# Performance work log

Hardware: AMD Instinct MI355X
Metric: run time of the kernel (lower is better)

The kernel has to match this reference:

```python
import jax, jax.numpy as jnp
import numpy as np

THRESHOLD = 0.9
N = 20000
K = 32
F = 64


def setup_inputs() -> dict:
    key = jax.random.key(0)
    k1, k2, k3, k4, k5 = jax.random.split(key, 5)
    features = jax.random.normal(k1, (N, F), dtype=jnp.float32)
    score = jax.random.normal(k2, (N, 1), dtype=jnp.float32)
    distances = jax.random.uniform(k3, (N, K), dtype=jnp.float32)
    # two equal segments; neighbours sampled within own segment, self at col 0
    row_splits = jnp.array([0, N // 2, N], dtype=jnp.int32)
    segN = N // 2
    local_self = (jnp.arange(N, dtype=jnp.int32) % segN)
    seg_start = (jnp.arange(N, dtype=jnp.int32) // segN) * segN
    r = jax.random.randint(k4, (N, K - 1), 0, segN - 1, dtype=jnp.int32)
    r = r + (r >= local_self[:, None]).astype(jnp.int32)  # avoid sampling self
    neigh = seg_start[:, None] + r
    nidxs = jnp.concatenate([jnp.arange(N, dtype=jnp.int32)[:, None], neigh], axis=1)
    tidxs = jax.random.randint(k5, (N, 1), 0, 50, dtype=jnp.int32)
    return {"features": features, "score": score, "distances": distances,
            "nidxs": nidxs, "row_splits": row_splits, "tidxs": tidxs}


def _lnc(features, score_logits, nidxs, row_splits):
    n, k = nidxs.shape
    score = jax.nn.sigmoid(score_logits[:, 0])  # [N]
    # hierarchy order: per row-split segment, descending score
    seg_id = jnp.searchsorted(row_splits, jnp.arange(n), side='right') - 1
    order = jnp.lexsort((-score, seg_id))

    arangeK = jnp.arange(k)

    def step(carry, p):
        ggather, sel, npg, gcount = carry
        already = ggather[p] >= 0
        high = score[p] > THRESHOLD
        m = nidxs[p]                                   # [K], m[0] == p (self)
        free = (m >= 0) & (ggather[jnp.clip(m, 0, n - 1)] < 0)
        self_only = arangeK == 0
        valid = jnp.where(high, free, self_only) & (~already) & (m >= 0)
        g = gcount
        idx_w = jnp.where(valid, m, n)                 # dummy slot n for masked writes
        ggather = ggather.at[idx_w].set(g)
        row_i = jnp.where(already, n, g)
        sel = sel.at[row_i].set(jnp.where(valid, m, -1))
        npg = npg.at[row_i].set(jnp.sum(valid.astype(jnp.int32)))
        created = (~already).astype(jnp.int32)
        return (ggather, sel, npg, gcount + created), created

    init = (jnp.full((n + 1,), -1, jnp.int32),
            jnp.full((n + 1, k), -1, jnp.int32),
            jnp.zeros((n + 1,), jnp.int32),
            jnp.int32(0))
    (ggather, sel, npg, gcount), created = jax.lax.scan(step, init, order)
    ggather, sel, npg = ggather[:n], sel[:n], npg[:n]

    # new row splits: cumulative group count at segment boundaries
    cum = jnp.cumsum(created)
    rs_new = jnp.concatenate([jnp.zeros((1,), jnp.int32),
                              cum[row_splits[1:] - 1].astype(jnp.int32)])

    # pooled features per group (rows >= gcount are padding)
    sel_c = jnp.clip(sel, 0, n - 1)
    gathered = features[sel_c]                         # [N, K, F]
    mask = (sel >= 0)[..., None]
    out_mean = jnp.sum(jnp.where(mask, gathered, 0.0), axis=1)
    out_mean = out_mean / (npg[:, None].astype(features.dtype) + 1e-6)
    out_max = jnp.max(jnp.where(mask, gathered, -1000.0), axis=1)
    out = jnp.concatenate([out_mean, out_max], axis=-1)  # [N, 2F]
    backgather = ggather[:, None]
    return out, rs_new, backgather


def reference(features, score, distances, nidxs, row_splits, tidxs):
    # distances/tidxs only feed the (disabled) loss branch; kept for signature parity
    return _lnc(features, score, nidxs, row_splits)
```

## Files before the change

### kernel.cpp

```cpp
#include <hip/hip_runtime.h>


constexpr int KN = 32;
constexpr int FD = 64;
constexpr int HOCAP = 512;
constexpr int EW = 16;
constexpr int NBB = 2048;
constexpr int NT = 256;
constexpr int NMAX = 20000;
constexpr int BSLOT = 64;
constexpr int TS = 2048;

typedef unsigned long long u64;

__device__ __forceinline__ int swz(int i) { return i ^ ((i >> 4) & 3); }

__global__ void k0_init(const float* __restrict__ score, float* __restrict__ s,
                        int* __restrict__ grab, u64* __restrict__ hlkStage,
                        int* __restrict__ hcnt, int* __restrict__ lcnt0,
                        int* __restrict__ lcnt1, u64* __restrict__ key,
                        const int* __restrict__ row_splits, int n) {
  __shared__ int ch, cl0, cl1;
  int tid = (int)threadIdx.x, bid = (int)blockIdx.x;
  int x = bid * NT + tid;
  int lane = tid & 63;
  int half = row_splits[1];
  if (tid == 0) { ch = 0; cl0 = 0; cl1 = 0; }
  __syncthreads();
  bool hi = false, lo = false;
  u64 pk = 0;
  if (x < n) {
    float sp = 1.0f / (1.0f + expf(-score[x]));
    s[x] = sp; grab[x] = 0x7FFFFFFF;
    hi = sp > 0.9f; lo = !hi;
    unsigned sb = __float_as_uint(sp);
    pk = ((u64)(x >= half) << 63) | ((u64)(0x7FFFFFFFu - sb) << 32) | (unsigned)x;
    key[x] = lo ? (((u64)sb << 32) | (u64)(0xFFFFFFFFu - (unsigned)x)) : 0ull;
  }
  u64 bh = __ballot(hi);
  u64 b0 = __ballot(lo && x < half);
  u64 b1 = __ballot(lo && x >= half);
  int base = 0;
  if (lane == 0) {
    if (bh) base = atomicAdd(&ch, __popcll(bh));
    if (b0) atomicAdd(&cl0, __popcll(b0));
    if (b1) atomicAdd(&cl1, __popcll(b1));
  }
  base = __shfl(base, 0);
  if (hi) {
    int idx = base + __popcll(bh & ((1ull << lane) - 1ull));
    if (idx < BSLOT) hlkStage[bid * BSLOT + idx] = pk;
  }
  __syncthreads();
  if (tid == 0) {
    hcnt[bid] = (ch > BSLOT) ? BSLOT : ch;
    lcnt0[bid] = cl0; lcnt1[bid] = cl1;
  }
}

__global__ __launch_bounds__(1024, 1) void kA(
    const u64* __restrict__ hlkStage, const int* __restrict__ hcnt,
    const int* __restrict__ lcnt0, const int* __restrict__ lcnt1,
    const int* __restrict__ nidxs, const int* __restrict__ row_splits,
    int* __restrict__ nbm, int* __restrict__ fgj, int* __restrict__ counters,
    int n) {
  __shared__ unsigned short hr16[NMAX];
  __shared__ unsigned E[HOCAP * EW];
  __shared__ u64 hk[HOCAP];
  __shared__ int hol[HOCAP];
  __shared__ int fgjL[HOCAP];
  __shared__ int cnts[128];
  __shared__ int pref[129];
  __shared__ int lsum[2];
  __shared__ int shg;
  int tid = (int)threadIdx.x;
  int lane = tid & 63;
  int half = row_splits[1];
  int nblk = (n + NT - 1) / NT; if (nblk > 128) nblk = 128;

  {
    unsigned* h32 = (unsigned*)hr16;
    for (int i = tid; i < NMAX / 2; i += 1024) h32[i] = 0xFFFFFFFFu;
  }
  for (int i = tid; i < HOCAP * EW; i += 1024) E[i] = 0u;
  if (tid < 128) cnts[tid] = (tid < nblk) ? hcnt[tid] : 0;
  if (tid == 0) { lsum[0] = 0; lsum[1] = 0; }
  __syncthreads();

  if (tid < 64) {
    int v0 = cnts[tid], v1 = cnts[64 + tid];
#pragma unroll
    for (int off = 1; off < 64; off <<= 1) {
      int t0 = __shfl_up(v0, off), t1 = __shfl_up(v1, off);
      if (lane >= off) { v0 += t0; v1 += t1; }
    }
    int s0 = __shfl(v0, 63);
    pref[tid + 1] = v0;
    pref[64 + tid + 1] = v1 + s0;
    if (tid == 0) pref[0] = 0;
  }
  if (tid >= 64 && tid < 192) {
    int b = tid - 64;
    if (b < nblk) { atomicAdd(&lsum[0], lcnt0[b]); atomicAdd(&lsum[1], lcnt1[b]); }
  }
  __syncthreads();
  int nh = pref[nblk]; if (nh > HOCAP) nh = HOCAP;

  for (int t = tid; t < nblk * BSLOT; t += 1024) {
    int b = t >> 6, j = t & (BSLOT - 1);
    if (j < cnts[b]) {
      int d = pref[b] + j;
      if (d < HOCAP) hk[d] = hlkStage[t];
    }
  }
  __syncthreads();

  for (int i = tid; i < nh; i += 1024) {
    u64 kp = hk[i];
    int rk = 0;
#pragma unroll 8
    for (int j = 0; j < nh; ++j) rk += (hk[j] < kp) ? 1 : 0;
    int p = (int)(unsigned)(kp & 0xFFFFFFFFu);
    hol[rk] = p; hr16[p] = (unsigned short)rk;
  }
  __syncthreads();

  {
    const int4* nsrc = (const int4*)nidxs;
    int4* ndstG = (int4*)nbm;
    int tot = nh * 8;
    for (int t = tid; t < tot; t += 1024) {
      int j = t >> 3, q4 = t & 7;
      int p = hol[j];
      int4 v = nsrc[p * 8 + q4];
      ndstG[t] = v;
      unsigned bit = 1u << (j & 31);
      unsigned widx = (unsigned)(j >> 5);
      int xs[4] = { v.x, v.y, v.z, v.w };
#pragma unroll
      for (int e = 0; e < 4; ++e) {
        unsigned r = ((unsigned)xs[e] < (unsigned)n) ? hr16[xs[e]] : 0xFFFFu;
        if (r != 0xFFFFu) atomicOr(&E[r * EW + widx], bit);
      }
    }
  }
  __syncthreads();

  if (tid < 64) {
    unsigned Fw[16];
#pragma unroll
    for (int w = 0; w < 16; ++w) Fw[w] = 0u;
    int hg = 0, h0 = 0, h1 = 0;
    u64 mask_lt = (1ull << lane) - 1ull;
#pragma unroll
    for (int c = 0; c < HOCAP / 64; ++c) {
      if (c * 64 >= nh) break;
      int j = c * 64 + lane;
      bool valid = j < nh;
      unsigned er[16];
#pragma unroll
      for (int w = 0; w < 16; ++w) er[w] = valid ? E[j * EW + w] : 0u;
      unsigned acc = 0;
#pragma unroll
      for (int w = 0; w < 16; ++w) acc |= er[w] & Fw[w];
      bool base_already = acc != 0u;
      u64 erc = ((u64)er[2 * c + 1] << 32) | er[2 * c];
      u64 fb = 0;
      for (int l = 0; l < 64; ++l) {
        bool already = base_already || ((erc & fb) != 0ull);
        bool formed = valid && !already;
        fb |= __ballot(formed && (lane == l));
      }
      Fw[2 * c]     |= (unsigned)(fb & 0xFFFFFFFFull);
      Fw[2 * c + 1] |= (unsigned)(fb >> 32);
      bool formed = (fb >> lane) & 1ull;
      int p = valid ? hol[j] : 0;
      if (formed) {
        int idx = hg + __popcll(fb & mask_lt);
        fgjL[idx] = j;
      }
      h0 += __popcll(__ballot(formed && p < half));
      h1 += __popcll(__ballot(formed && p >= half));
      hg += __popcll(fb);
    }
    if (lane == 0) {
      counters[1] = hg; counters[2] = h0; counters[3] = h1; shg = hg;
    }
  }
  __syncthreads();
  int hg = shg;
  for (int i = tid; i < hg; i += 1024) fgj[i] = fgjL[i];
  if (tid == 0) {
    counters[0] = nh;
    counters[4] = lsum[0];
    counters[5] = lsum[1];
  }
}

__global__ void kG(const float* __restrict__ s, const int* __restrict__ nbm,
                   const int* __restrict__ fgj, int* __restrict__ grab,
                   u64* __restrict__ key, int* __restrict__ counters,
                   const int* __restrict__ row_splits, int n) {
  int t = (int)(blockIdx.x * blockDim.x + threadIdx.x);
  int lane = (int)threadIdx.x & 63;
  int half = row_splits[1];
  int hg = counters[1];
  bool gl0 = false, gl1 = false;
  if (t < hg * KN) {
    int g = t >> 5;
    int x = nbm[fgj[g] * KN + (t & 31)];
    if ((unsigned)x < (unsigned)n) {
      int old = atomicMin(&grab[x], g);
      if (old == 0x7FFFFFFF && !(s[x] > 0.9f)) {
        key[x] = 0ull;
        if (x < half) gl0 = true; else gl1 = true;
      }
    }
  }
  u64 b0 = __ballot(gl0), b1 = __ballot(gl1);
  if (lane == 0) {
    if (b0) atomicSub(&counters[4], __popcll(b0));
    if (b1) atomicSub(&counters[5], __popcll(b1));
  }
}

__global__ void kBC(const int* __restrict__ row_splits, const u64* __restrict__ key,
                    const int* __restrict__ grab, const int* __restrict__ nbm,
                    const int* __restrict__ fgj, const int* __restrict__ counters,
                    const float* __restrict__ feat, float* __restrict__ out,
                    int n, int rs_off) {
  __shared__ u64 ktile[TS];
  int tid = (int)threadIdx.x, bid = (int)blockIdx.x;
  int gtid = bid * NT + tid;
  int lane = tid & 63;
  int wv = tid >> 6;
  int half = row_splits[1];
  const int GSZ = NBB * NT;
  const int NW = GSZ >> 6;
  int wid = gtid >> 6;
  int hg = counters[1], H0 = counters[2], H1 = counters[3];
  int L0 = counters[4], L1 = counters[5];
  int G = H0 + H1 + L0 + L1;
  int bg = rs_off + 3;
  const float inv1 = 1.0f / (1.0f + 1e-6f);

  for (int x = gtid; x < n; x += GSZ) {
    int prov = grab[x];
    if (prov != 0x7FFFFFFF)
      out[bg + x] = (float)((prov < H0) ? prov : (prov + L0));
  }

  for (int row = G + wid; row < n; row += NW) {
    out[row * (2 * FD) + lane] = 0.0f;
    out[row * (2 * FD) + FD + lane] = -1000.0f;
  }

  {
    int wtail = (NBB - 1 - bid) * (NT >> 6) + wv;
    for (int g = wtail; g < hg; g += NW) {
      int x = 0;
      bool mine = false;
      if (lane < KN) {
        x = nbm[fgj[g] * KN + lane];
        mine = (grab[x] == g);
      }
      u64 bal = __ballot(mine);
      unsigned mask = (unsigned)(bal & 0xFFFFFFFFull);
      int npg = __popc(mask);
      float sum = 0.0f, mx = -1000.0f;
      for (int k = 0; k < KN; ++k) {
        if (mask & (1u << k)) {
          int m = __shfl(x, k);
          float v = feat[m * FD + lane];
          sum += v; mx = fmaxf(mx, v);
        }
      }
      int gid2 = (g < H0) ? g : (g + L0);
      out[gid2 * (2 * FD) + lane] = sum / ((float)npg + 1e-6f);
      out[gid2 * (2 * FD) + FD + lane] = mx;
    }
  }

  int nblk16 = (n + 15) >> 4;
  for (int tsk = bid; tsk < nblk16; tsk += NBB) {
    int p0 = tsk * 16;
    int pw = p0 + wv * 4;
    u64 kp[4];
#pragma unroll
    for (int j = 0; j < 4; ++j) kp[j] = (pw + j < n) ? key[pw + j] : 0ull;
    int seg_lo = (p0 < half) ? 0 : half;
    int seg_cnt = (p0 < half) ? half : (n - half);
    unsigned r0 = 0, r1 = 0, r2 = 0, r3 = 0;
    for (int toff = 0; toff < seg_cnt; toff += TS) {
      int tcnt = seg_cnt - toff; if (tcnt > TS) tcnt = TS;
      __syncthreads();
      for (int i = tid; i < tcnt; i += NT) ktile[swz(i)] = key[seg_lo + toff + i];
      __syncthreads();
      for (int i = lane; i < tcnt; i += 64) {
        u64 kk = ktile[swz(i)];
        r0 += (kk > kp[0]) ? 1u : 0u;
        r1 += (kk > kp[1]) ? 1u : 0u;
        r2 += (kk > kp[2]) ? 1u : 0u;
        r3 += (kk > kp[3]) ? 1u : 0u;
      }
    }
#pragma unroll
    for (int off = 32; off > 0; off >>= 1) {
      r0 += __shfl_down(r0, off);
      r1 += __shfl_down(r1, off);
      r2 += __shfl_down(r2, off);
      r3 += __shfl_down(r3, off);
    }
    r0 = __shfl(r0, 0); r1 = __shfl(r1, 0); r2 = __shfl(r2, 0); r3 = __shfl(r3, 0);
    unsigned rr[4] = { r0, r1, r2, r3 };
#pragma unroll
    for (int j = 0; j < 4; ++j) {
      if (kp[j] == 0ull) continue;
      int p = pw + j;
      int base = (p < half) ? H0 : (H0 + L0 + H1);
      int gid = base + (int)rr[j];
      float v = feat[p * FD + lane];
      out[gid * (2 * FD) + lane] = v * inv1;
      out[gid * (2 * FD) + FD + lane] = v;
      if (lane == 0) out[bg + p] = (float)gid;
    }
  }

  if (gtid == 0) {
    out[rs_off + 0] = 0.0f;
    out[rs_off + 1] = (float)(H0 + L0);
    out[rs_off + 2] = (float)(H0 + L0 + H1 + L1);
  }
}

extern "C" void kernel_launch(void* const* d_in, const int* in_sizes, int n_in,
                              void* d_out, int out_size, void* d_ws, size_t ws_size,
                              hipStream_t stream) {
  const float* features   = (const float*)d_in[0];
  const float* score      = (const float*)d_in[1];
  const int*   nidxs      = (const int*)d_in[3];
  const int*   row_splits = (const int*)d_in[4];
  int n = in_sizes[1];
  float* out = (float*)d_out;
  int* wsi = (int*)d_ws;
  int rs_off = n * 2 * FD;

  int*      counters = wsi;
  float*    s        = (float*)(wsi + 8);
  int*      grab     = wsi + 8 + n;
  u64*      key      = (u64*)(wsi + 8 + 2 * n);
  int*      nbm      = wsi + 8 + 5 * n;
  int*      fgj      = wsi + 8 + 5 * n + HOCAP * KN;
  u64*      hlkStage = (u64*)(fgj + 2 * HOCAP);
  int*      hcnt     = (int*)(hlkStage + 128 * BSLOT);
  int*      lcnt0    = hcnt + 128;
  int*      lcnt1    = lcnt0 + 128;

  int blocks = (n + NT - 1) / NT;
  k0_init<<<blocks, NT, 0, stream>>>(score, s, grab, hlkStage, hcnt, lcnt0,
                                     lcnt1, key, row_splits, n);
  kA<<<1, 1024, 0, stream>>>(hlkStage, hcnt, lcnt0, lcnt1, nidxs, row_splits,
                             nbm, fgj, counters, n);
  kG<<<(HOCAP * KN) / NT, NT, 0, stream>>>(s, nbm, fgj, grab, key, counters,
                                           row_splits, n);
  kBC<<<NBB, NT, 0, stream>>>(row_splits, key, grab, nbm, fgj, counters,
                              features, out, n, rs_off);
}
```

Baseline: 69.99 us.

## Drop score buffer, shrink kA block, reorder kBC phases

Removes the separate sigmoid score buffer and has kG test whether the key is nonzero to detect low-score points, which saves one global write and one read. Reduces the single-block kA launch from 1024 to 512 threads. Moves the backgather, padding and high-group pooling loops in kBC after the rank-based low-score placement loop, so the heavy ranking work starts first. Each change is small, and together they touch several kernels.

```diff
diff --git a/kernel.cpp b/kernel.cpp
--- a/kernel.cpp
+++ b/kernel.cpp
@@ -7,6 +7,7 @@
 constexpr int EW = 16;
 constexpr int NBB = 2048;
 constexpr int NT = 256;
+constexpr int NTA = 512;
 constexpr int NMAX = 20000;
 constexpr int BSLOT = 64;
 constexpr int TS = 2048;
@@ -15,11 +16,11 @@
 
 __device__ __forceinline__ int swz(int i) { return i ^ ((i >> 4) & 3); }
 
-__global__ void k0_init(const float* __restrict__ score, float* __restrict__ s,
-                        int* __restrict__ grab, u64* __restrict__ hlkStage,
-                        int* __restrict__ hcnt, int* __restrict__ lcnt0,
-                        int* __restrict__ lcnt1, u64* __restrict__ key,
-                        const int* __restrict__ row_splits, int n) {
+__global__ void k0_init(const float* __restrict__ score, int* __restrict__ grab,
+                        u64* __restrict__ hlkStage, int* __restrict__ hcnt,
+                        int* __restrict__ lcnt0, int* __restrict__ lcnt1,
+                        u64* __restrict__ key, const int* __restrict__ row_splits,
+                        int n) {
   __shared__ int ch, cl0, cl1;
   int tid = (int)threadIdx.x, bid = (int)blockIdx.x;
   int x = bid * NT + tid;
@@ -31,7 +32,7 @@
   u64 pk = 0;
   if (x < n) {
     float sp = 1.0f / (1.0f + expf(-score[x]));
-    s[x] = sp; grab[x] = 0x7FFFFFFF;
+    grab[x] = 0x7FFFFFFF;
     hi = sp > 0.9f; lo = !hi;
     unsigned sb = __float_as_uint(sp);
     pk = ((u64)(x >= half) << 63) | ((u64)(0x7FFFFFFFu - sb) << 32) | (unsigned)x;
@@ -58,7 +59,7 @@
   }
 }
 
-__global__ __launch_bounds__(1024, 1) void kA(
+__global__ __launch_bounds__(NTA, 1) void kA(
     const u64* __restrict__ hlkStage, const int* __restrict__ hcnt,
     const int* __restrict__ lcnt0, const int* __restrict__ lcnt1,
     const int* __restrict__ nidxs, const int* __restrict__ row_splits,
@@ -80,9 +81,9 @@
 
   {
     unsigned* h32 = (unsigned*)hr16;
-    for (int i = tid; i < NMAX / 2; i += 1024) h32[i] = 0xFFFFFFFFu;
-  }
-  for (int i = tid; i < HOCAP * EW; i += 1024) E[i] = 0u;
+    for (int i = tid; i < NMAX / 2; i += NTA) h32[i] = 0xFFFFFFFFu;
+  }
+  for (int i = tid; i < HOCAP * EW; i += NTA) E[i] = 0u;
   if (tid < 128) cnts[tid] = (tid < nblk) ? hcnt[tid] : 0;
   if (tid == 0) { lsum[0] = 0; lsum[1] = 0; }
   __syncthreads();
@@ -106,7 +107,7 @@
   __syncthreads();
   int nh = pref[nblk]; if (nh > HOCAP) nh = HOCAP;
 
-  for (int t = tid; t < nblk * BSLOT; t += 1024) {
+  for (int t = tid; t < nblk * BSLOT; t += NTA) {
     int b = t >> 6, j = t & (BSLOT - 1);
     if (j < cnts[b]) {
       int d = pref[b] + j;
@@ -115,7 +116,7 @@
   }
   __syncthreads();
 
-  for (int i = tid; i < nh; i += 1024) {
+  for (int i = tid; i < nh; i += NTA) {
     u64 kp = hk[i];
     int rk = 0;
 #pragma unroll 8
@@ -129,7 +130,7 @@
     const int4* nsrc = (const int4*)nidxs;
     int4* ndstG = (int4*)nbm;
     int tot = nh * 8;
-    for (int t = tid; t < tot; t += 1024) {
+    for (int t = tid; t < tot; t += NTA) {
       int j = t >> 3, q4 = t & 7;
       int p = hol[j];
       int4 v = nsrc[p * 8 + q4];
@@ -189,7 +190,7 @@
   }
   __syncthreads();
   int hg = shg;
-  for (int i = tid; i < hg; i += 1024) fgj[i] = fgjL[i];
+  for (int i = tid; i < hg; i += NTA) fgj[i] = fgjL[i];
   if (tid == 0) {
     counters[0] = nh;
     counters[4] = lsum[0];
@@ -197,10 +198,10 @@
   }
 }
 
-__global__ void kG(const float* __restrict__ s, const int* __restrict__ nbm,
-                   const int* __restrict__ fgj, int* __restrict__ grab,
-                   u64* __restrict__ key, int* __restrict__ counters,
-                   const int* __restrict__ row_splits, int n) {
+__global__ void kG(const int* __restrict__ nbm, const int* __restrict__ fgj,
+                   int* __restrict__ grab, u64* __restrict__ key,
+                   int* __restrict__ counters, const int* __restrict__ row_splits,
+                   int n) {
   int t = (int)(blockIdx.x * blockDim.x + threadIdx.x);
   int lane = (int)threadIdx.x & 63;
   int half = row_splits[1];
@@ -211,7 +212,7 @@
     int x = nbm[fgj[g] * KN + (t & 31)];
     if ((unsigned)x < (unsigned)n) {
       int old = atomicMin(&grab[x], g);
-      if (old == 0x7FFFFFFF && !(s[x] > 0.9f)) {
+      if (old == 0x7FFFFFFF && key[x] != 0ull) {
         key[x] = 0ull;
         if (x < half) gl0 = true; else gl1 = true;
       }
@@ -244,43 +245,6 @@
   int bg = rs_off + 3;
   const float inv1 = 1.0f / (1.0f + 1e-6f);
 
-  for (int x = gtid; x < n; x += GSZ) {
-    int prov = grab[x];
-    if (prov != 0x7FFFFFFF)
-      out[bg + x] = (float)((prov < H0) ? prov : (prov + L0));
-  }
-
-  for (int row = G + wid; row < n; row += NW) {
-    out[row * (2 * FD) + lane] = 0.0f;
-    out[row * (2 * FD) + FD + lane] = -1000.0f;
-  }
-
-  {
-    int wtail = (NBB - 1 - bid) * (NT >> 6) + wv;
-    for (int g = wtail; g < hg; g += NW) {
-      int x = 0;
-      bool mine = false;
-      if (lane < KN) {
-        x = nbm[fgj[g] * KN + lane];
-        mine = (grab[x] == g);
-      }
-      u64 bal = __ballot(mine);
-      unsigned mask = (unsigned)(bal & 0xFFFFFFFFull);
-      int npg = __popc(mask);
-      float sum = 0.0f, mx = -1000.0f;
-      for (int k = 0; k < KN; ++k) {
-        if (mask & (1u << k)) {
-          int m = __shfl(x, k);
-          float v = feat[m * FD + lane];
-          sum += v; mx = fmaxf(mx, v);
-        }
-      }
-      int gid2 = (g < H0) ? g : (g + L0);
-      out[gid2 * (2 * FD) + lane] = sum / ((float)npg + 1e-6f);
-      out[gid2 * (2 * FD) + FD + lane] = mx;
-    }
-  }
-
   int nblk16 = (n + 15) >> 4;
   for (int tsk = bid; tsk < nblk16; tsk += NBB) {
     int p0 = tsk * 16;
@@ -326,6 +290,43 @@
     }
   }
 
+  for (int x = gtid; x < n; x += GSZ) {
+    int prov = grab[x];
+    if (prov != 0x7FFFFFFF)
+      out[bg + x] = (float)((prov < H0) ? prov : (prov + L0));
+  }
+
+  for (int row = G + wid; row < n; row += NW) {
+    out[row * (2 * FD) + lane] = 0.0f;
+    out[row * (2 * FD) + FD + lane] = -1000.0f;
+  }
+
+  {
+    int wtail = (NBB - 1 - bid) * (NT >> 6) + wv;
+    for (int g = wtail; g < hg; g += NW) {
+      int x = 0;
+      bool mine = false;
+      if (lane < KN) {
+        x = nbm[fgj[g] * KN + lane];
+        mine = (grab[x] == g);
+      }
+      u64 bal = __ballot(mine);
+      unsigned mask = (unsigned)(bal & 0xFFFFFFFFull);
+      int npg = __popc(mask);
+      float sum = 0.0f, mx = -1000.0f;
+      for (int k = 0; k < KN; ++k) {
+        if (mask & (1u << k)) {
+          int m = __shfl(x, k);
+          float v = feat[m * FD + lane];
+          sum += v; mx = fmaxf(mx, v);
+        }
+      }
+      int gid2 = (g < H0) ? g : (g + L0);
+      out[gid2 * (2 * FD) + lane] = sum / ((float)npg + 1e-6f);
+      out[gid2 * (2 * FD) + FD + lane] = mx;
+    }
+  }
+
   if (gtid == 0) {
     out[rs_off + 0] = 0.0f;
     out[rs_off + 1] = (float)(H0 + L0);
@@ -346,7 +347,6 @@
   int rs_off = n * 2 * FD;
 
   int*      counters = wsi;
-  float*    s        = (float*)(wsi + 8);
   int*      grab     = wsi + 8 + n;
   u64*      key      = (u64*)(wsi + 8 + 2 * n);
   int*      nbm      = wsi + 8 + 5 * n;
@@ -357,11 +357,11 @@
   int*      lcnt1    = lcnt0 + 128;
 
   int blocks = (n + NT - 1) / NT;
-  k0_init<<<blocks, NT, 0, stream>>>(score, s, grab, hlkStage, hcnt, lcnt0,
+  k0_init<<<blocks, NT, 0, stream>>>(score, grab, hlkStage, hcnt, lcnt0,
                                      lcnt1, key, row_splits, n);
-  kA<<<1, 1024, 0, stream>>>(hlkStage, hcnt, lcnt0, lcnt1, nidxs, row_splits,
-                             nbm, fgj, counters, n);
-  kG<<<(HOCAP * KN) / NT, NT, 0, stream>>>(s, nbm, fgj, grab, key, counters,
+  kA<<<1, NTA, 0, stream>>>(hlkStage, hcnt, lcnt0, lcnt1, nidxs, row_splits,
+                            nbm, fgj, counters, n);
+  kG<<<(HOCAP * KN) / NT, NT, 0, stream>>>(nbm, fgj, grab, key, counters,
                                            row_splits, n);
   kBC<<<NBB, NT, 0, stream>>>(row_splits, key, grab, nbm, fgj, counters,
                               features, out, n, rs_off);
```

Measured after the change: 72.80 us. +4.0%, slower.
